# Kernel tuning notes

Measured on AMD Instinct MI355X. Metric: run time of the kernel, lower is better.

The kernel has to match this reference:

```python
import jax, jax.numpy as jnp
import numpy as np

VOCAB, EMBED, HIDDEN = 32000, 512, 1024
BATCH, MAX_LEN = 128, 48


def setup_inputs() -> dict:
    key = jax.random.key(0)
    ks = jax.random.split(key, 9)
    s = 0.02
    return {
        "encoder_h": jax.random.normal(ks[0], (BATCH, HIDDEN), jnp.float32),
        "encoder_c": jax.random.normal(ks[1], (BATCH, HIDDEN), jnp.float32),
        "embedding": jax.random.normal(ks[2], (VOCAB, EMBED), jnp.float32) * s,
        "w_ih": jax.random.normal(ks[3], (4 * HIDDEN, EMBED), jnp.float32) * s,
        "w_hh": jax.random.normal(ks[4], (4 * HIDDEN, HIDDEN), jnp.float32) * s,
        "b_ih": jax.random.normal(ks[5], (4 * HIDDEN,), jnp.float32) * s,
        "b_hh": jax.random.normal(ks[6], (4 * HIDDEN,), jnp.float32) * s,
        "w_out": jax.random.normal(ks[7], (VOCAB, HIDDEN), jnp.float32) * s,
        "b_out": jax.random.normal(ks[8], (VOCAB,), jnp.float32) * s,
        "sos_id": 1,
        "max_len": MAX_LEN,
    }


def reference(encoder_h, encoder_c, embedding, w_ih, w_hh, b_ih, b_hh,
              w_out, b_out, sos_id, max_len):
    batch = encoder_h.shape[0]
    vocab = w_out.shape[0]
    bias = b_ih + b_hh  # [4H]

    def step(carry, _):
        h, c, x = carry  # h,c: [B,H], x: [B,E]
        gates = x @ w_ih.T + h @ w_hh.T + bias          # [B,4H]
        i_g, f_g, g_g, o_g = jnp.split(gates, 4, axis=-1)  # torch order i,f,g,o
        i_g = jax.nn.sigmoid(i_g)
        f_g = jax.nn.sigmoid(f_g)
        g_g = jnp.tanh(g_g)
        o_g = jax.nn.sigmoid(o_g)
        c = f_g * c + i_g * g_g
        h = o_g * jnp.tanh(c)
        logits = h @ w_out.T + b_out                    # [B,V]
        top1 = jnp.argmax(logits, axis=1)               # greedy next token
        x = embedding[top1]                             # [B,E]
        return (h, c, x), logits

    x0 = jnp.broadcast_to(embedding[sos_id], (batch, embedding.shape[1]))
    init = (encoder_h, encoder_c, x0)
    _, logits_seq = jax.lax.scan(step, init, None, length=max_len - 1)  # [T-1,B,V]
    # outputs[0] stays zeros, as in the torch code
    zeros0 = jnp.zeros((1, batch, vocab), logits_seq.dtype)
    return jnp.concatenate([zeros0, logits_seq], axis=0)  # [max_len,B,V]
```

## Files before the change

kernel.cpp:

```cpp
#include <hip/hip_runtime.h>
#include <math.h>


typedef unsigned short u16;
typedef unsigned int u32;
typedef __bf16 bf16x8 __attribute__((ext_vector_type(8)));
typedef float f32x4 __attribute__((ext_vector_type(4)));

#define B_ 128
#define E_ 512
#define H_ 1024
#define V_ 32000
#define G4 4096
#define KX 1536

__device__ __forceinline__ u16 f2bf(float f){
  u32 u = __float_as_uint(f);
  u32 r = (u + 0x7FFFu + ((u >> 16) & 1u)) >> 16;
  return (u16)r;
}
__device__ __forceinline__ float bf2f(u16 s){ return __uint_as_float(((u32)s) << 16); }
__device__ __forceinline__ void split3(float x, u16 &a, u16 &b, u16 &c){
  a = f2bf(x); float r1 = x - bf2f(a);
  b = f2bf(r1); float r2 = r1 - bf2f(b);
  c = f2bf(r2);
}
__device__ __forceinline__ bf16x8 ldb8(const u16* p){ return *reinterpret_cast<const bf16x8*>(p); }
__device__ __forceinline__ f32x4 mf(bf16x8 a, bf16x8 b, f32x4 c){
  return __builtin_amdgcn_mfma_f32_16x16x32_bf16(a, b, c, 0, 0, 0);
}


__global__ void k_zero(float* __restrict__ p){
  const int i = blockIdx.x * 256 + threadIdx.x;
  reinterpret_cast<float4*>(p)[i] = make_float4(0.f, 0.f, 0.f, 0.f);
}

__global__ void k_wout(const float* __restrict__ w, u16* __restrict__ wo){
  const int i = blockIdx.x * 256 + threadIdx.x;
  float4 v = reinterpret_cast<const float4*>(w)[i];
  ushort4 o;
  o.x = f2bf(v.x); o.y = f2bf(v.y); o.z = f2bf(v.z); o.w = f2bf(v.w);
  reinterpret_cast<ushort4*>(wo)[i] = o;
}

__global__ void k_wc(const float* __restrict__ wih, const float* __restrict__ whh,
                     u16* __restrict__ ch, u16* __restrict__ cm, u16* __restrict__ cl){
  const int k = blockIdx.x * 256 + threadIdx.x;
  const int n = blockIdx.y;
  float v = (k < E_) ? wih[(size_t)n * E_ + k] : whh[(size_t)n * H_ + (k - E_)];
  u16 a, b, c; split3(v, a, b, c);
  const size_t o = (size_t)n * KX + k;
  ch[o] = a; cm[o] = b; cl[o] = c;
}

__global__ void k_xh0(const float* __restrict__ emb, const float* __restrict__ ench,
                      const int* __restrict__ sos,
                      u16* __restrict__ xh, u16* __restrict__ xm, u16* __restrict__ xl){
  const int k = blockIdx.x * 256 + threadIdx.x;
  const int m = blockIdx.y;
  float v = (k < E_) ? emb[(size_t)sos[0] * E_ + k] : ench[(size_t)m * H_ + (k - E_)];
  u16 a, b, c; split3(v, a, b, c);
  const int o = m * KX + k;
  xh[o] = a; xm[o] = b; xl[o] = c;
}

__global__ void k_c0(const float* __restrict__ src, float* __restrict__ dst){
  const int i = blockIdx.x * 256 + threadIdx.x;
  dst[i] = src[i];
}


__global__ __launch_bounds__(64) void k_gates(
    const u16* __restrict__ xh_h, const u16* __restrict__ xh_m, const u16* __restrict__ xh_l,
    const u16* __restrict__ wc_h, const u16* __restrict__ wc_m, const u16* __restrict__ wc_l,
    float* __restrict__ part){
  const int L = threadIdx.x;
  const u32 bid = blockIdx.x;
  const int w  = bid & 3;
  const int nb = (bid >> 2) & 63;
  const int mb = (int)(bid >> 8);
  const int l15 = L & 15, q = L >> 4;
  const int kb = w * 384 + q * 8;

  const u16* pa[3] = { xh_h, xh_m, xh_l };
  const u16* pb[3] = { wc_h, wc_m, wc_l };

  f32x4 acc[4][4];
  const f32x4 z4 = {0.f, 0.f, 0.f, 0.f};
#pragma unroll
  for (int i = 0; i < 4; ++i)
#pragma unroll
    for (int g = 0; g < 4; ++g) acc[i][g] = z4;

  const int arow0 = mb * 64 + l15;
  const int brow0 = nb * 16 + l15;

#pragma unroll 1
  for (int it = 0; it < 6; ++it){
#pragma unroll
    for (int kc = 0; kc < 2; ++kc){
      const int ko = kb + it * 64 + kc * 32;
      bf16x8 af[4][3], bfr[4][3];
#pragma unroll
      for (int i = 0; i < 4; ++i)
#pragma unroll
        for (int s = 0; s < 3; ++s)
          af[i][s] = ldb8(pa[s] + (size_t)(arow0 + i * 16) * KX + ko);
#pragma unroll
      for (int g = 0; g < 4; ++g)
#pragma unroll
        for (int s = 0; s < 3; ++s)
          bfr[g][s] = ldb8(pb[s] + (size_t)(g * 1024 + brow0) * KX + ko);
#pragma unroll
      for (int i = 0; i < 4; ++i)
#pragma unroll
        for (int g = 0; g < 4; ++g){
          f32x4 a_ = acc[i][g];
          a_ = mf(af[i][0], bfr[g][0], a_);
          a_ = mf(af[i][0], bfr[g][1], a_);
          a_ = mf(af[i][1], bfr[g][0], a_);
          a_ = mf(af[i][0], bfr[g][2], a_);
          a_ = mf(af[i][1], bfr[g][1], a_);
          a_ = mf(af[i][2], bfr[g][0], a_);
          acc[i][g] = a_;
        }
    }
  }
#pragma unroll
  for (int i = 0; i < 4; ++i)
#pragma unroll
    for (int g = 0; g < 4; ++g)
#pragma unroll
      for (int r = 0; r < 4; ++r){
        const int row = mb * 64 + i * 16 + q * 4 + r;
        const int col = g * 1024 + nb * 16 + l15;
        part[(size_t)(w * B_ + row) * G4 + col] = acc[i][g][r];
      }
}

__global__ __launch_bounds__(256) void k_cell(
    const float* __restrict__ part, const float* __restrict__ bih, const float* __restrict__ bhh,
    float* __restrict__ c_f, float* __restrict__ h_f,
    u16* __restrict__ xh_h, u16* __restrict__ xh_m, u16* __restrict__ xh_l){
  const int idx = blockIdx.x * 256 + threadIdx.x;
  const int m = idx >> 10, u = idx & 1023;
  float gi = bih[u] + bhh[u];
  float gf = bih[1024 + u] + bhh[1024 + u];
  float gg = bih[2048 + u] + bhh[2048 + u];
  float go = bih[3072 + u] + bhh[3072 + u];
#pragma unroll
  for (int s = 0; s < 4; ++s){
    const float* p = part + (size_t)(s * B_ + m) * G4 + u;
    gi += p[0]; gf += p[1024]; gg += p[2048]; go += p[3072];
  }
  const float ig = 1.f / (1.f + expf(-gi));
  const float fg = 1.f / (1.f + expf(-gf));
  const float g2 = tanhf(gg);
  const float og = 1.f / (1.f + expf(-go));
  const float c = fg * c_f[idx] + ig * g2;
  c_f[idx] = c;
  const float h = og * tanhf(c);
  h_f[idx] = h;
  u16 a, b, cc; split3(h, a, b, cc);
  const int o = m * KX + E_ + u;
  xh_h[o] = a; xh_m[o] = b; xh_l[o] = cc;
}

__global__ __launch_bounds__(256) void k_logits(
    const u16* __restrict__ xh_h, const u16* __restrict__ wo,
    const float* __restrict__ bout, float* __restrict__ out, int t){
  __shared__ alignas(16) u16 lA[128 * 72];
  const int tid = threadIdx.x;
  const int L = tid & 63, wv = tid >> 6;
  const int l15 = L & 15, q = L >> 4;
  const int C0 = blockIdx.x * 128;

  f32x4 acc[8][2];
  const f32x4 z4 = {0.f, 0.f, 0.f, 0.f};
#pragma unroll
  for (int i = 0; i < 8; ++i){ acc[i][0] = z4; acc[i][1] = z4; }

  const u16* bptr0 = wo + (size_t)(C0 + wv * 32 + l15) * H_ + q * 8;
  const u16* bptr1 = bptr0 + (size_t)16 * H_;

#pragma unroll 1
  for (int it = 0; it < 16; ++it){
    const int k0 = it * 64;
#pragma unroll
    for (int s2 = 0; s2 < 4; ++s2){
      const int c = tid + 256 * s2;
      const int row = c >> 3, ch = c & 7;
      *reinterpret_cast<uint4*>(&lA[row * 72 + ch * 8]) =
        *reinterpret_cast<const uint4*>(&xh_h[(size_t)row * KX + E_ + k0 + ch * 8]);
    }
    __syncthreads();
    const bf16x8 b00 = ldb8(bptr0 + k0);
    const bf16x8 b01 = ldb8(bptr0 + k0 + 32);
    const bf16x8 b10 = ldb8(bptr1 + k0);
    const bf16x8 b11 = ldb8(bptr1 + k0 + 32);
#pragma unroll
    for (int i = 0; i < 8; ++i){
      const bf16x8 a0 = ldb8(&lA[(i * 16 + l15) * 72 + q * 8]);
      const bf16x8 a1 = ldb8(&lA[(i * 16 + l15) * 72 + 32 + q * 8]);
      acc[i][0] = mf(a0, b00, acc[i][0]);
      acc[i][0] = mf(a1, b01, acc[i][0]);
      acc[i][1] = mf(a0, b10, acc[i][1]);
      acc[i][1] = mf(a1, b11, acc[i][1]);
    }
    __syncthreads();
  }
  const size_t ob = (size_t)t * B_ * V_;
#pragma unroll
  for (int j = 0; j < 2; ++j){
    const int n = C0 + wv * 32 + j * 16 + l15;
    const float bo = bout[n];
#pragma unroll
    for (int i = 0; i < 8; ++i)
#pragma unroll
      for (int r = 0; r < 4; ++r){
        const int m = i * 16 + q * 4 + r;
        out[ob + (size_t)m * V_ + n] = acc[i][j][r] + bo;
      }
  }
}

__global__ __launch_bounds__(256) void k_argmax(
    const float* __restrict__ out, int t,
    const float* __restrict__ h_f, const float* __restrict__ w_out,
    const float* __restrict__ bout, const float* __restrict__ emb,
    u16* __restrict__ xh_h, u16* __restrict__ xh_m, u16* __restrict__ xh_l){
  __shared__ float cv[512];
  __shared__ int   ci[512];
  __shared__ int   sel_i[8];
  __shared__ double refv[8];
  __shared__ int   s_tok;
  const int m = blockIdx.x, tid = threadIdx.x;
  const float* row = out + (size_t)t * B_ * V_ + (size_t)m * V_;

  float v1 = -1e38f, v2 = -1e38f; int i1 = 0, i2 = 0;
  for (int n = tid; n < V_; n += 256){
    const float v = row[n];
    if (v > v1){ v2 = v1; i2 = i1; v1 = v; i1 = n; }
    else if (v > v2){ v2 = v; i2 = n; }
  }
  cv[tid] = v1; ci[tid] = i1; cv[256 + tid] = v2; ci[256 + tid] = i2;
  __syncthreads();

  for (int s = 0; s < 8; ++s){
    if (tid < 64){
      float bv = -1e38f; int bp = 0;
#pragma unroll
      for (int qq = 0; qq < 8; ++qq){
        const int p = tid * 8 + qq;
        const float v = cv[p];
        if (v > bv){ bv = v; bp = p; }
      }
      for (int off = 32; off >= 1; off >>= 1){
        const float ov = __shfl_xor(bv, off);
        const int   op = __shfl_xor(bp, off);
        if (ov > bv || (ov == bv && op < bp)){ bv = ov; bp = op; }
      }
      if (tid == 0) sel_i[s] = ci[bp];
      if ((bp >> 3) == tid) cv[bp] = -1e38f;
    }
    __syncthreads();
  }

  {
    const int wv = tid >> 6, L = tid & 63;
    const int c = wv * 2 + (L >> 5);
    const int kk = L & 31;
    const int idx = sel_i[c];
    const float* hr = h_f + (size_t)m * H_;
    const float* wr = w_out + (size_t)idx * H_;
    double a = 0.0;
#pragma unroll 4
    for (int qq = 0; qq < 32; ++qq){
      const int k = qq * 32 + kk;
      a += (double)hr[k] * (double)wr[k];
    }
    for (int off = 16; off >= 1; off >>= 1) a += __shfl_xor(a, off);
    if (kk == 0) refv[c] = a + (double)bout[idx];
  }
  __syncthreads();

  if (tid == 0){
    double bb = -1e300; int bi = 0x7fffffff;
#pragma unroll
    for (int c = 0; c < 8; ++c){
      const double v = refv[c]; const int idx = sel_i[c];
      if (v > bb || (v == bb && idx < bi)){ bb = v; bi = idx; }
    }
    s_tok = bi;
  }
  __syncthreads();

  const int tok = s_tok;
  for (int k = tid; k < E_; k += 256){
    const float v = emb[(size_t)tok * E_ + k];
    u16 a, b, c2; split3(v, a, b, c2);
    const int o = m * KX + k;
    xh_h[o] = a; xh_m[o] = b; xh_l[o] = c2;
  }
}


extern "C" void kernel_launch(void* const* d_in, const int* in_sizes, int n_in,
                              void* d_out, int out_size, void* d_ws, size_t ws_size,
                              hipStream_t stream){
  const float* enc_h = (const float*)d_in[0];
  const float* enc_c = (const float*)d_in[1];
  const float* emb   = (const float*)d_in[2];
  const float* w_ih  = (const float*)d_in[3];
  const float* w_hh  = (const float*)d_in[4];
  const float* b_ih  = (const float*)d_in[5];
  const float* b_hh  = (const float*)d_in[6];
  const float* w_out = (const float*)d_in[7];
  const float* b_out = (const float*)d_in[8];
  const int*   sos   = (const int*)d_in[9];
  float* out = (float*)d_out;

  char* ws = (char*)d_ws;
  const size_t XH_SZ = (size_t)B_ * KX * 2;
  const size_t WC_SZ = (size_t)G4 * KX * 2;
  const size_t WO_SZ = (size_t)V_ * H_ * 2;
  const size_t PT_SZ = (size_t)4 * B_ * G4 * 4;
  const size_t HC_SZ = (size_t)B_ * H_ * 4;
  u16* xh_h = (u16*)ws; ws += XH_SZ;
  u16* xh_m = (u16*)ws; ws += XH_SZ;
  u16* xh_l = (u16*)ws; ws += XH_SZ;
  u16* wc_h = (u16*)ws; ws += WC_SZ;
  u16* wc_m = (u16*)ws; ws += WC_SZ;
  u16* wc_l = (u16*)ws; ws += WC_SZ;
  u16* wo   = (u16*)ws; ws += WO_SZ;
  float* part = (float*)ws; ws += PT_SZ;
  float* h_f  = (float*)ws; ws += HC_SZ;
  float* c_f  = (float*)ws; ws += HC_SZ;

  k_zero<<<4000, 256, 0, stream>>>(out);
  k_wout<<<32000, 256, 0, stream>>>(w_out, wo);
  k_wc<<<dim3(6, 4096), 256, 0, stream>>>(w_ih, w_hh, wc_h, wc_m, wc_l);
  k_xh0<<<dim3(6, 128), 256, 0, stream>>>(emb, enc_h, sos, xh_h, xh_m, xh_l);
  k_c0<<<512, 256, 0, stream>>>(enc_c, c_f);

  for (int t = 1; t < 48; ++t){
    k_gates<<<512, 64, 0, stream>>>(xh_h, xh_m, xh_l, wc_h, wc_m, wc_l, part);
    k_cell<<<512, 256, 0, stream>>>(part, b_ih, b_hh, c_f, h_f, xh_h, xh_m, xh_l);
    k_logits<<<250, 256, 0, stream>>>(xh_h, wo, b_out, out, t);
    if (t < 47)
      k_argmax<<<128, 256, 0, stream>>>(out, t, h_f, w_out, b_out, emb,
                                        xh_h, xh_m, xh_l);
  }
}
```

Baseline: 6.066 ms.

## Fuse gate GEMM with LSTM cell and emit top-2 candidates from logits

The gate GEMM and LSTM cell update now run in one kernel. Each block reduces its split-K partials through shared memory and applies the nonlinearities in place, so the global partials buffer and the separate cell launch are gone. The hidden-state split buffers are double-buffered so the fused kernel can write the next state while other blocks still read the current one. The logits kernel also reduces each row to a per-wave top-2 candidate list, so argmax scans 2000 candidates instead of re-reading 32000 logits per row. This adds shuffle work to the logits epilogue and changes the gate tiling to 256 blocks of 4 waves.

```diff
diff --git a/kernel.cpp b/kernel.cpp
--- a/kernel.cpp
+++ b/kernel.cpp
@@ -13,6 +13,7 @@
 #define V_ 32000
 #define G4 4096
 #define KX 1536
+#define NC 2000
 
 __device__ __forceinline__ u16 f2bf(float f){
   u32 u = __float_as_uint(f);
@@ -71,105 +72,106 @@
 }
 
 
-__global__ __launch_bounds__(64) void k_gates(
+__global__ __launch_bounds__(256) void k_gates_cell(
     const u16* __restrict__ xh_h, const u16* __restrict__ xh_m, const u16* __restrict__ xh_l,
     const u16* __restrict__ wc_h, const u16* __restrict__ wc_m, const u16* __restrict__ wc_l,
-    float* __restrict__ part){
-  const int L = threadIdx.x;
-  const u32 bid = blockIdx.x;
-  const int w  = bid & 3;
-  const int nb = (bid >> 2) & 63;
-  const int mb = (int)(bid >> 8);
+    const float* __restrict__ bih, const float* __restrict__ bhh,
+    float* __restrict__ c_f, float* __restrict__ h_f,
+    u16* __restrict__ oh, u16* __restrict__ om, u16* __restrict__ ol){
+  __shared__ float red[4][64 * 33];
+  const int tid = threadIdx.x;
+  const int L = tid & 63, w = tid >> 6;
   const int l15 = L & 15, q = L >> 4;
-  const int kb = w * 384 + q * 8;
+  const int mb = (int)blockIdx.x & 1;
+  const int ub = (int)blockIdx.x >> 1;
 
   const u16* pa[3] = { xh_h, xh_m, xh_l };
   const u16* pb[3] = { wc_h, wc_m, wc_l };
 
-  f32x4 acc[4][4];
+  f32x4 acc[4][2];
   const f32x4 z4 = {0.f, 0.f, 0.f, 0.f};
 #pragma unroll
-  for (int i = 0; i < 4; ++i)
-#pragma unroll
-    for (int g = 0; g < 4; ++g) acc[i][g] = z4;
+  for (int i = 0; i < 4; ++i){ acc[i][0] = z4; acc[i][1] = z4; }
 
   const int arow0 = mb * 64 + l15;
-  const int brow0 = nb * 16 + l15;
+  const size_t brow[2] = {
+    (size_t)(((l15 >> 3)) * 1024 + ub * 8 + (l15 & 7)),
+    (size_t)((2 + (l15 >> 3)) * 1024 + ub * 8 + (l15 & 7)) };
+  const int kb = w * 384 + q * 8;
 
 #pragma unroll 1
   for (int it = 0; it < 6; ++it){
 #pragma unroll
     for (int kc = 0; kc < 2; ++kc){
       const int ko = kb + it * 64 + kc * 32;
-      bf16x8 af[4][3], bfr[4][3];
+      bf16x8 af[4][3], bfr[2][3];
 #pragma unroll
       for (int i = 0; i < 4; ++i)
 #pragma unroll
         for (int s = 0; s < 3; ++s)
           af[i][s] = ldb8(pa[s] + (size_t)(arow0 + i * 16) * KX + ko);
 #pragma unroll
-      for (int g = 0; g < 4; ++g)
+      for (int ct = 0; ct < 2; ++ct)
 #pragma unroll
         for (int s = 0; s < 3; ++s)
-          bfr[g][s] = ldb8(pb[s] + (size_t)(g * 1024 + brow0) * KX + ko);
+          bfr[ct][s] = ldb8(pb[s] + brow[ct] * KX + ko);
 #pragma unroll
       for (int i = 0; i < 4; ++i)
 #pragma unroll
-        for (int g = 0; g < 4; ++g){
-          f32x4 a_ = acc[i][g];
-          a_ = mf(af[i][0], bfr[g][0], a_);
-          a_ = mf(af[i][0], bfr[g][1], a_);
-          a_ = mf(af[i][1], bfr[g][0], a_);
-          a_ = mf(af[i][0], bfr[g][2], a_);
-          a_ = mf(af[i][1], bfr[g][1], a_);
-          a_ = mf(af[i][2], bfr[g][0], a_);
-          acc[i][g] = a_;
+        for (int ct = 0; ct < 2; ++ct){
+          f32x4 a_ = acc[i][ct];
+          a_ = mf(af[i][0], bfr[ct][0], a_);
+          a_ = mf(af[i][0], bfr[ct][1], a_);
+          a_ = mf(af[i][1], bfr[ct][0], a_);
+          a_ = mf(af[i][0], bfr[ct][2], a_);
+          a_ = mf(af[i][1], bfr[ct][1], a_);
+          a_ = mf(af[i][2], bfr[ct][0], a_);
+          acc[i][ct] = a_;
         }
     }
   }
 #pragma unroll
   for (int i = 0; i < 4; ++i)
 #pragma unroll
-    for (int g = 0; g < 4; ++g)
-#pragma unroll
-      for (int r = 0; r < 4; ++r){
-        const int row = mb * 64 + i * 16 + q * 4 + r;
-        const int col = g * 1024 + nb * 16 + l15;
-        part[(size_t)(w * B_ + row) * G4 + col] = acc[i][g][r];
-      }
-}
-
-__global__ __launch_bounds__(256) void k_cell(
-    const float* __restrict__ part, const float* __restrict__ bih, const float* __restrict__ bhh,
-    float* __restrict__ c_f, float* __restrict__ h_f,
-    u16* __restrict__ xh_h, u16* __restrict__ xh_m, u16* __restrict__ xh_l){
-  const int idx = blockIdx.x * 256 + threadIdx.x;
-  const int m = idx >> 10, u = idx & 1023;
-  float gi = bih[u] + bhh[u];
-  float gf = bih[1024 + u] + bhh[1024 + u];
-  float gg = bih[2048 + u] + bhh[2048 + u];
-  float go = bih[3072 + u] + bhh[3072 + u];
-#pragma unroll
-  for (int s = 0; s < 4; ++s){
-    const float* p = part + (size_t)(s * B_ + m) * G4 + u;
-    gi += p[0]; gf += p[1024]; gg += p[2048]; go += p[3072];
-  }
-  const float ig = 1.f / (1.f + expf(-gi));
-  const float fg = 1.f / (1.f + expf(-gf));
-  const float g2 = tanhf(gg);
-  const float og = 1.f / (1.f + expf(-go));
-  const float c = fg * c_f[idx] + ig * g2;
-  c_f[idx] = c;
-  const float h = og * tanhf(c);
-  h_f[idx] = h;
-  u16 a, b, cc; split3(h, a, b, cc);
-  const int o = m * KX + E_ + u;
-  xh_h[o] = a; xh_m[o] = b; xh_l[o] = cc;
+    for (int ct = 0; ct < 2; ++ct)
+#pragma unroll
+      for (int r = 0; r < 4; ++r)
+        red[w][(i * 16 + q * 4 + r) * 33 + ct * 16 + l15] = acc[i][ct][r];
+  __syncthreads();
+
+#pragma unroll
+  for (int rep = 0; rep < 2; ++rep){
+    const int idx = tid + rep * 256;
+    const int ml = idx >> 3, uu = idx & 7;
+    float gv[4];
+#pragma unroll
+    for (int g = 0; g < 4; ++g){
+      const int c = (g >> 1) * 16 + ((g & 1) << 3) + uu;
+      const float s = red[0][ml * 33 + c] + red[1][ml * 33 + c]
+                    + red[2][ml * 33 + c] + red[3][ml * 33 + c];
+      const int n = g * 1024 + ub * 8 + uu;
+      gv[g] = s + bih[n] + bhh[n];
+    }
+    const float ig = 1.f / (1.f + expf(-gv[0]));
+    const float fg = 1.f / (1.f + expf(-gv[1]));
+    const float g2 = tanhf(gv[2]);
+    const float og = 1.f / (1.f + expf(-gv[3]));
+    const int mg = mb * 64 + ml, ug = ub * 8 + uu;
+    const int ci_ = mg * H_ + ug;
+    const float c = fg * c_f[ci_] + ig * g2;
+    c_f[ci_] = c;
+    const float h = og * tanhf(c);
+    h_f[ci_] = h;
+    u16 a, b, cc; split3(h, a, b, cc);
+    const int o = mg * KX + E_ + ug;
+    oh[o] = a; om[o] = b; ol[o] = cc;
+  }
 }
 
 __global__ __launch_bounds__(256) void k_logits(
     const u16* __restrict__ xh_h, const u16* __restrict__ wo,
-    const float* __restrict__ bout, float* __restrict__ out, int t){
+    const float* __restrict__ bout, float* __restrict__ out,
+    float2* __restrict__ cand, int t){
   __shared__ alignas(16) u16 lA[128 * 72];
   const int tid = threadIdx.x;
   const int L = tid & 63, wv = tid >> 6;
@@ -211,22 +213,40 @@
     __syncthreads();
   }
   const size_t ob = (size_t)t * B_ * V_;
-#pragma unroll
-  for (int j = 0; j < 2; ++j){
-    const int n = C0 + wv * 32 + j * 16 + l15;
-    const float bo = bout[n];
-#pragma unroll
-    for (int i = 0; i < 8; ++i)
-#pragma unroll
-      for (int r = 0; r < 4; ++r){
-        const int m = i * 16 + q * 4 + r;
-        out[ob + (size_t)m * V_ + n] = acc[i][j][r] + bo;
+  const int n0 = C0 + wv * 32 + l15;
+  const float bo0 = bout[n0], bo1 = bout[n0 + 16];
+  const int cw = (int)blockIdx.x * 4 + wv;
+#pragma unroll
+  for (int i = 0; i < 8; ++i)
+#pragma unroll
+    for (int r = 0; r < 4; ++r){
+      const int m = i * 16 + q * 4 + r;
+      const float va = acc[i][0][r] + bo0;
+      const float vb = acc[i][1][r] + bo1;
+      out[ob + (size_t)m * V_ + n0] = va;
+      out[ob + (size_t)m * V_ + n0 + 16] = vb;
+      float v1, v2; int i1, i2;
+      if (va >= vb){ v1 = va; i1 = n0;      v2 = vb; i2 = n0 + 16; }
+      else         { v1 = vb; i1 = n0 + 16; v2 = va; i2 = n0; }
+#pragma unroll
+      for (int mm = 1; mm <= 8; mm <<= 1){
+        const float ov1 = __shfl_xor(v1, mm), ov2 = __shfl_xor(v2, mm);
+        const int   oi1 = __shfl_xor(i1, mm), oi2 = __shfl_xor(i2, mm);
+        if (ov1 > v1){
+          if (v1 >= ov2){ v2 = v1; i2 = i1; } else { v2 = ov2; i2 = oi2; }
+          v1 = ov1; i1 = oi1;
+        } else if (ov1 > v2){ v2 = ov1; i2 = oi1; }
       }
-  }
+      if (l15 == 0){
+        float2* crow = cand + (size_t)m * NC;
+        crow[cw]        = make_float2(v1, __int_as_float(i1));
+        crow[1000 + cw] = make_float2(v2, __int_as_float(i2));
+      }
+    }
 }
 
 __global__ __launch_bounds__(256) void k_argmax(
-    const float* __restrict__ out, int t,
+    const float2* __restrict__ cand,
     const float* __restrict__ h_f, const float* __restrict__ w_out,
     const float* __restrict__ bout, const float* __restrict__ emb,
     u16* __restrict__ xh_h, u16* __restrict__ xh_m, u16* __restrict__ xh_l){
@@ -236,13 +256,14 @@
   __shared__ double refv[8];
   __shared__ int   s_tok;
   const int m = blockIdx.x, tid = threadIdx.x;
-  const float* row = out + (size_t)t * B_ * V_ + (size_t)m * V_;
+  const float2* cr = cand + (size_t)m * NC;
 
   float v1 = -1e38f, v2 = -1e38f; int i1 = 0, i2 = 0;
-  for (int n = tid; n < V_; n += 256){
-    const float v = row[n];
-    if (v > v1){ v2 = v1; i2 = i1; v1 = v; i1 = n; }
-    else if (v > v2){ v2 = v; i2 = n; }
+  for (int n = tid; n < NC; n += 256){
+    const float2 e = cr[n];
+    const float v = e.x; const int ii = __float_as_int(e.y);
+    if (v > v1){ v2 = v1; i2 = i1; v1 = v; i1 = ii; }
+    else if (v > v2){ v2 = v; i2 = ii; }
   }
   cv[tid] = v1; ci[tid] = i1; cv[256 + tid] = v2; ci[256 + tid] = i2;
   __syncthreads();
@@ -325,31 +346,37 @@
   const size_t XH_SZ = (size_t)B_ * KX * 2;
   const size_t WC_SZ = (size_t)G4 * KX * 2;
   const size_t WO_SZ = (size_t)V_ * H_ * 2;
-  const size_t PT_SZ = (size_t)4 * B_ * G4 * 4;
+  const size_t CD_SZ = (size_t)B_ * NC * 8;
   const size_t HC_SZ = (size_t)B_ * H_ * 4;
-  u16* xh_h = (u16*)ws; ws += XH_SZ;
-  u16* xh_m = (u16*)ws; ws += XH_SZ;
-  u16* xh_l = (u16*)ws; ws += XH_SZ;
+  u16* X_h[2]; u16* X_m[2]; u16* X_l[2];
+  X_h[0] = (u16*)ws; ws += XH_SZ;
+  X_m[0] = (u16*)ws; ws += XH_SZ;
+  X_l[0] = (u16*)ws; ws += XH_SZ;
+  X_h[1] = (u16*)ws; ws += XH_SZ;
+  X_m[1] = (u16*)ws; ws += XH_SZ;
+  X_l[1] = (u16*)ws; ws += XH_SZ;
   u16* wc_h = (u16*)ws; ws += WC_SZ;
   u16* wc_m = (u16*)ws; ws += WC_SZ;
   u16* wc_l = (u16*)ws; ws += WC_SZ;
   u16* wo   = (u16*)ws; ws += WO_SZ;
-  float* part = (float*)ws; ws += PT_SZ;
+  float2* cand = (float2*)ws; ws += CD_SZ;
   float* h_f  = (float*)ws; ws += HC_SZ;
   float* c_f  = (float*)ws; ws += HC_SZ;
 
   k_zero<<<4000, 256, 0, stream>>>(out);
   k_wout<<<32000, 256, 0, stream>>>(w_out, wo);
   k_wc<<<dim3(6, 4096), 256, 0, stream>>>(w_ih, w_hh, wc_h, wc_m, wc_l);
-  k_xh0<<<dim3(6, 128), 256, 0, stream>>>(emb, enc_h, sos, xh_h, xh_m, xh_l);
+  k_xh0<<<dim3(6, 128), 256, 0, stream>>>(emb, enc_h, sos, X_h[0], X_m[0], X_l[0]);
   k_c0<<<512, 256, 0, stream>>>(enc_c, c_f);
 
   for (int t = 1; t < 48; ++t){
-    k_gates<<<512, 64, 0, stream>>>(xh_h, xh_m, xh_l, wc_h, wc_m, wc_l, part);
-    k_cell<<<512, 256, 0, stream>>>(part, b_ih, b_hh, c_f, h_f, xh_h, xh_m, xh_l);
-    k_logits<<<250, 256, 0, stream>>>(xh_h, wo, b_out, out, t);
+    const int d = t & 1, s = d ^ 1;
+    k_gates_cell<<<256, 256, 0, stream>>>(X_h[s], X_m[s], X_l[s],
+                                          wc_h, wc_m, wc_l, b_ih, b_hh,
+                                          c_f, h_f, X_h[d], X_m[d], X_l[d]);
+    k_logits<<<250, 256, 0, stream>>>(X_h[d], wo, b_out, out, cand, t);
     if (t < 47)
-      k_argmax<<<128, 256, 0, stream>>>(out, t, h_f, w_out, b_out, emb,
-                                        xh_h, xh_m, xh_l);
-  }
-}
+      k_argmax<<<128, 256, 0, stream>>>(cand, h_f, w_out, b_out, emb,
+                                        X_h[d], X_m[d], X_l[d]);
+  }
+}
```

Result: faster. 5.010 ms (-17.4%).
